# Kernel tuning notes

Hardware: AMD Instinct MI355X
Metric: run time of the kernel (lower is better)

## Reference

```python
import jax, jax.numpy as jnp
import numpy as np

H, W, D = 512, 512, 16
THETA_ALPHA, THETA_BETA, THETA_GAMMA = 160.0, 3.0, 3.0
NUM_ITERS = 5
SPATIAL_RADIUS = 9      # ~3*theta_gamma truncation for the Gaussian spatial kernel
BILATERAL_RADIUS = 2    # small window stand-in for the permutohedral bilateral filter


def _gauss1d(sigma, radius):
    x = jnp.arange(-radius, radius + 1, dtype=jnp.float32)
    return jnp.exp(-(x * x) / (2.0 * sigma * sigma))  # unnormalized; norm-vals divide cancels scale


def spatial_filter(x):
    # x: (d, h, w) -> depthwise separable Gaussian blur with sigma = theta_gamma
    k = _gauss1d(THETA_GAMMA, SPATIAL_RADIUS)
    xi = x[:, None]  # (d, 1, h, w): d acts as batch, single channel
    kh = k.reshape(1, 1, -1, 1)
    kw = k.reshape(1, 1, 1, -1)
    y = jax.lax.conv_general_dilated(xi, kh, (1, 1), [(SPATIAL_RADIUS, SPATIAL_RADIUS), (0, 0)])
    y = jax.lax.conv_general_dilated(y, kw, (1, 1), [(0, 0), (SPATIAL_RADIUS, SPATIAL_RADIUS)])
    return y[:, 0]


def bilateral_filter(x, rgb):
    # x: (d, h, w), rgb: (3, h, w). Windowed bilateral (joint spatial/color Gaussian),
    # a dense stand-in for the permutohedral-lattice high_dim_filter custom op.
    d, h, w = x.shape
    r = BILATERAL_RADIUS
    xp = jnp.pad(x, ((0, 0), (r, r), (r, r)))
    rp = jnp.pad(rgb, ((0, 0), (r, r), (r, r)))
    vp = jnp.pad(jnp.ones((h, w), x.dtype), ((r, r), (r, r)))
    inv2a = 1.0 / (2.0 * THETA_ALPHA * THETA_ALPHA)
    inv2b = 1.0 / (2.0 * THETA_BETA * THETA_BETA)
    out = jnp.zeros_like(x)
    for dy in range(-r, r + 1):
        for dx in range(-r, r + 1):  # fixed small offset set, not a data-dim loop
            xs = xp[:, r + dy:r + dy + h, r + dx:r + dx + w]
            rs = rp[:, r + dy:r + dy + h, r + dx:r + dx + w]
            vs = vp[r + dy:r + dy + h, r + dx:r + dx + w]
            wgt = jnp.exp(-(dy * dy + dx * dx) * inv2a
                          - jnp.sum((rgb - rs) ** 2, axis=0) * inv2b) * vs
            out = out + wgt[None] * xs
    return out


def setup_inputs() -> dict:
    key = jax.random.key(0)
    ks = jax.random.split(key, 8)
    eye = jnp.eye(D, dtype=jnp.float32)
    return {
        "image": jax.random.uniform(ks[0], (1, H, W, 3), jnp.float32) * 255.0,
        "unaries_box": jax.random.normal(ks[1], (1, D, H, W), jnp.float32),
        "unaries_global": jax.random.normal(ks[2], (1, D, H, W), jnp.float32),
        "spatial_ker_weights": eye + 0.05 * jax.random.normal(ks[3], (D, D), jnp.float32),
        "bilateral_ker_weights": eye + 0.05 * jax.random.normal(ks[4], (D, D), jnp.float32),
        "compatibility_matrix": -eye + 0.05 * jax.random.normal(ks[5], (D, D), jnp.float32),
        "box_weight": jax.random.uniform(ks[6], (1,), jnp.float32),
        "global_weight": jax.random.uniform(ks[7], (1,), jnp.float32),
    }


def reference(image, unaries_box, unaries_global, spatial_ker_weights,
              bilateral_ker_weights, compatibility_matrix, box_weight, global_weight):
    unaries = unaries_box[0] * box_weight + unaries_global[0] * global_weight  # (d, h, w)
    rgb = jnp.transpose(image[0], (2, 0, 1))  # (3, h, w)

    ones = jnp.ones((D, H, W), jnp.float32)
    spatial_norm = spatial_filter(ones)
    bilateral_norm = bilateral_filter(ones, rgb)

    q = unaries
    for _ in range(NUM_ITERS):
        p = jax.nn.softmax(q, axis=0)                       # over detections
        sp = spatial_filter(p) / spatial_norm
        bl = bilateral_filter(p, rgb) / bilateral_norm
        msg = (jnp.einsum('ij,jhw->ihw', spatial_ker_weights, sp)
               + jnp.einsum('ij,jhw->ihw', bilateral_ker_weights, bl))
        pairwise = jnp.einsum('ij,jhw->ihw', compatibility_matrix, msg)
        q = unaries - pairwise

    return jnp.transpose(q, (1, 2, 0))[None]  # (1, h, w, d)
```

## Files before the change

kernel.cpp:

```cpp
#include <hip/hip_runtime.h>


constexpr int H = 512, W = 512;
constexpr int HW = H * W;
constexpr int NUM_ITERS = 5;
constexpr float INV2A = 1.0f / (2.0f * 160.0f * 160.0f);
constexpr float INV2B = 1.0f / (2.0f * 3.0f * 3.0f);

constexpr size_t PLANAR_F = (size_t)HW * 8;
constexpr size_t OFF_U  = 0;
constexpr size_t OFF_PA = OFF_U  + (size_t)HW * 16;
constexpr size_t OFF_PB = OFF_PA + PLANAR_F;
constexpr size_t OFF_T  = OFF_PB + PLANAR_F;
constexpr size_t OFF_SV = OFF_T  + PLANAR_F;
constexpr size_t OFF_KG = OFF_SV + 512;
constexpr size_t OFF_M1 = OFF_KG + 32;
constexpr size_t OFF_M2 = OFF_M1 + 256;

__device__ inline void unpack2(unsigned u, float& lo, float& hi) {
    lo = __uint_as_float(u << 16);
    hi = __uint_as_float(u & 0xFFFF0000u);
}
__device__ inline unsigned short f2bf(float x) {
    unsigned u = __float_as_uint(x);
    return (unsigned short)((u + 0x7FFFu + ((u >> 16) & 1u)) >> 16);
}
__device__ inline unsigned pack2(float a, float b) {
    return (unsigned)f2bf(a) | ((unsigned)f2bf(b) << 16);
}
__device__ inline int swz8(int b, int per) { return (b & 7) * per + (b >> 3); }

__global__ void k_init(const float* __restrict__ Sw, const float* __restrict__ Bw,
                       const float* __restrict__ Cm, float* __restrict__ ws) {
    __shared__ float kg[19];
    int tid = threadIdx.x;
    if (tid < 19) { int t = tid - 9; kg[tid] = expf(-(float)(t * t) / 18.0f); }
    __syncthreads();
    if (tid < 19) ws[OFF_KG + tid] = kg[tid];
    if (tid < 512) {
        float s = 0.0f;
        for (int t = -9; t <= 9; ++t) {
            int yy = tid + t;
            if (yy >= 0 && yy < 512) s += kg[t + 9];
        }
        ws[OFF_SV + tid] = s;
    }
    if (tid < 256) {
        int r = tid >> 4, c = tid & 15;
        float a = 0.0f, b = 0.0f;
        for (int k = 0; k < 16; ++k) {
            float cv = Cm[r * 16 + k];
            a += cv * Sw[k * 16 + c];
            b += cv * Bw[k * 16 + c];
        }
        ws[OFF_M1 + tid] = a;
        ws[OFF_M2 + tid] = b;
    }
}

__global__ __launch_bounds__(256) void k_prep(const float* __restrict__ ub,
                                              const float* __restrict__ ug,
                                              const float* __restrict__ pbw,
                                              const float* __restrict__ pgw,
                                              float* __restrict__ ws) {
    int pix = blockIdx.x * 256 + threadIdx.x;
    float bw = pbw[0], gw = pgw[0];

    float u[16];
#pragma unroll
    for (int i = 0; i < 16; ++i)
        u[i] = ub[(size_t)i * HW + pix] * bw + ug[(size_t)i * HW + pix] * gw;

    float4* U4 = (float4*)(ws + OFF_U);
#pragma unroll
    for (int j = 0; j < 4; ++j)
        U4[(size_t)pix * 4 + j] = make_float4(u[4 * j], u[4 * j + 1], u[4 * j + 2], u[4 * j + 3]);

    float m = u[0];
#pragma unroll
    for (int i = 1; i < 16; ++i) m = fmaxf(m, u[i]);
    float sum = 0.0f;
#pragma unroll
    for (int i = 0; i < 16; ++i) { u[i] = __expf(u[i] - m); sum += u[i]; }
    float inv = 1.0f / sum;
    uint2* PA = (uint2*)(ws + OFF_PA);
#pragma unroll
    for (int q = 0; q < 4; ++q)
        PA[(size_t)q * HW + pix] = make_uint2(pack2(u[4 * q] * inv, u[4 * q + 1] * inv),
                                              pack2(u[4 * q + 2] * inv, u[4 * q + 3] * inv));
}

__global__ __launch_bounds__(256) void k_convv(const float* __restrict__ ws,
                                               const uint2* __restrict__ P,
                                               uint2* __restrict__ T) {
    int b = swz8(blockIdx.x, 128);
    int gtid = b * 256 + threadIdx.x;
    int x  = gtid & 511;
    int q  = (gtid >> 9) & 3;
    int yb = (gtid >> 11) << 2;

    float kg[19];
#pragma unroll
    for (int t = 0; t < 19; ++t) kg[t] = ws[OFF_KG + t];

    const uint2* Pq = P + (size_t)q * HW;
    float4 acc[4];
#pragma unroll
    for (int k = 0; k < 4; ++k) acc[k] = make_float4(0.f, 0.f, 0.f, 0.f);

#pragma unroll
    for (int t = 0; t < 22; ++t) {
        int yy = yb + t - 9;
        float4 p = make_float4(0.f, 0.f, 0.f, 0.f);
        if ((unsigned)yy < (unsigned)H) {
            uint2 v = Pq[(size_t)yy * W + x];
            unpack2(v.x, p.x, p.y);
            unpack2(v.y, p.z, p.w);
        }
        int k0 = (t - 18 > 0) ? t - 18 : 0;
        int k1 = (t < 3) ? t : 3;
#pragma unroll
        for (int k = k0; k <= k1; ++k) {
            float w = kg[t - k];
            acc[k].x += w * p.x; acc[k].y += w * p.y;
            acc[k].z += w * p.z; acc[k].w += w * p.w;
        }
    }
    uint2* Tq = T + (size_t)q * HW;
#pragma unroll
    for (int k = 0; k < 4; ++k)
        Tq[(size_t)(yb + k) * W + x] = make_uint2(pack2(acc[k].x, acc[k].y),
                                                  pack2(acc[k].z, acc[k].w));
}

__global__ __launch_bounds__(256) void k_combine(const float* __restrict__ ws,
                                                 const float* __restrict__ img,
                                                 const uint2* __restrict__ Tsrc,
                                                 const uint2* __restrict__ Psrc,
                                                 uint2* __restrict__ Pdst,
                                                 float4* __restrict__ outF,
                                                 int do_softmax) {
    __shared__ uint2 sT[4 * 4 * 82];
    __shared__ uint2 sP[4 * 8 * 68];
    __shared__ float sI[8 * 68 * 3];
    __shared__ float skg[19];
    __shared__ float sM1[256], sM2[256];

    int tid = threadIdx.x;
    int b = swz8(blockIdx.x, 128);
    int x0 = (b & 7) * 64;
    int y0 = (b >> 3) * 4;

    if (tid < 19) skg[tid] = ws[OFF_KG + tid];
    sM1[tid] = ws[OFF_M1 + tid];
    sM2[tid] = ws[OFF_M2 + tid];

    for (int e = tid; e < 1312; e += 256) {
        int q = e / 328, rem = e - q * 328;
        int row = rem / 82, px = rem - row * 82;
        int gx = x0 - 9 + px;
        uint2 v = make_uint2(0u, 0u);
        if ((unsigned)gx < (unsigned)W)
            v = Tsrc[(size_t)q * HW + (size_t)(y0 + row) * W + gx];
        sT[e] = v;
    }
    for (int e = tid; e < 2176; e += 256) {
        int q = e / 544, rem = e - q * 544;
        int row = rem / 68, px = rem - row * 68;
        int gx = x0 - 2 + px, gy = y0 - 2 + row;
        uint2 v = make_uint2(0u, 0u);
        if ((unsigned)gx < (unsigned)W && (unsigned)gy < (unsigned)H)
            v = Psrc[(size_t)q * HW + (size_t)gy * W + gx];
        sP[e] = v;
    }
    for (int e = tid; e < 544; e += 256) {
        int row = e / 68, px = e - row * 68;
        int gx = x0 - 2 + px, gy = y0 - 2 + row;
        float r = 0.f, g = 0.f, bb = 0.f;
        if ((unsigned)gx < (unsigned)W && (unsigned)gy < (unsigned)H) {
            const float* ip = img + ((size_t)gy * W + gx) * 3;
            r = ip[0]; g = ip[1]; bb = ip[2];
        }
        sI[e * 3 + 0] = r; sI[e * 3 + 1] = g; sI[e * 3 + 2] = bb;
    }
    __syncthreads();

    int ly = tid >> 6, lx = tid & 63;
    int y = y0 + ly, x = x0 + lx;

    float qn[16];

    {
        float sp[16];
#pragma unroll
        for (int i = 0; i < 16; ++i) sp[i] = 0.0f;
#pragma unroll
        for (int t = 0; t < 19; ++t) {
            float k = skg[t];
            int base = ly * 82 + lx + t;
#pragma unroll
            for (int q = 0; q < 4; ++q) {
                uint2 v = sT[q * 328 + base];
                float a, bq, c, d;
                unpack2(v.x, a, bq); unpack2(v.y, c, d);
                sp[4 * q + 0] += k * a; sp[4 * q + 1] += k * bq;
                sp[4 * q + 2] += k * c; sp[4 * q + 3] += k * d;
            }
        }
        float inv_sn = 1.0f / (ws[OFF_SV + y] * ws[OFF_SV + x]);
#pragma unroll
        for (int i = 0; i < 16; ++i) sp[i] *= inv_sn;
#pragma unroll
        for (int i = 0; i < 16; ++i) {
            float acc = 0.0f;
#pragma unroll
            for (int j4 = 0; j4 < 4; ++j4) {
                float4 m1 = *(const float4*)&sM1[i * 16 + j4 * 4];
                acc += m1.x * sp[4 * j4 + 0] + m1.y * sp[4 * j4 + 1]
                     + m1.z * sp[4 * j4 + 2] + m1.w * sp[4 * j4 + 3];
            }
            qn[i] = -acc;
        }
    }

    {
        float bl[16];
#pragma unroll
        for (int i = 0; i < 16; ++i) bl[i] = 0.0f;
        float bn = 0.0f;
        const float* ic = &sI[((ly + 2) * 68 + lx + 2) * 3];
        float r0 = ic[0], g0 = ic[1], b0 = ic[2];
#pragma unroll
        for (int dy = 0; dy < 5; ++dy) {
            int gy = y + dy - 2;
            bool vy = (unsigned)gy < (unsigned)H;
#pragma unroll
            for (int dx = 0; dx < 5; ++dx) {
                int gx = x + dx - 2;
                const float* ip = &sI[((ly + dy) * 68 + lx + dx) * 3];
                float dr = r0 - ip[0], dg = g0 - ip[1], db = b0 - ip[2];
                float wgt = __expf(-(float)((dy - 2) * (dy - 2) + (dx - 2) * (dx - 2)) * INV2A
                                   - (dr * dr + dg * dg + db * db) * INV2B);
                if (!(vy && (unsigned)gx < (unsigned)W)) wgt = 0.0f;
                bn += wgt;
                int base = (ly + dy) * 68 + lx + dx;
#pragma unroll
                for (int q = 0; q < 4; ++q) {
                    uint2 v = sP[q * 544 + base];
                    float a, bq, c, d;
                    unpack2(v.x, a, bq); unpack2(v.y, c, d);
                    bl[4 * q + 0] += wgt * a; bl[4 * q + 1] += wgt * bq;
                    bl[4 * q + 2] += wgt * c; bl[4 * q + 3] += wgt * d;
                }
            }
        }
        float inv_bn = 1.0f / bn;
#pragma unroll
        for (int i = 0; i < 16; ++i) bl[i] *= inv_bn;
#pragma unroll
        for (int i = 0; i < 16; ++i) {
            float acc = 0.0f;
#pragma unroll
            for (int j4 = 0; j4 < 4; ++j4) {
                float4 m2 = *(const float4*)&sM2[i * 16 + j4 * 4];
                acc += m2.x * bl[4 * j4 + 0] + m2.y * bl[4 * j4 + 1]
                     + m2.z * bl[4 * j4 + 2] + m2.w * bl[4 * j4 + 3];
            }
            qn[i] -= acc;
        }
    }

    size_t pix = (size_t)y * W + x;
    const float4* U4 = (const float4*)(ws + OFF_U);
#pragma unroll
    for (int j = 0; j < 4; ++j) {
        float4 u = U4[pix * 4 + j];
        qn[4 * j + 0] += u.x; qn[4 * j + 1] += u.y;
        qn[4 * j + 2] += u.z; qn[4 * j + 3] += u.w;
    }

    if (do_softmax) {
        float m = qn[0];
#pragma unroll
        for (int i = 1; i < 16; ++i) m = fmaxf(m, qn[i]);
        float sum = 0.0f;
#pragma unroll
        for (int i = 0; i < 16; ++i) { qn[i] = __expf(qn[i] - m); sum += qn[i]; }
        float inv = 1.0f / sum;
#pragma unroll
        for (int q = 0; q < 4; ++q)
            Pdst[(size_t)q * HW + pix] = make_uint2(pack2(qn[4 * q] * inv, qn[4 * q + 1] * inv),
                                                    pack2(qn[4 * q + 2] * inv, qn[4 * q + 3] * inv));
    } else {
#pragma unroll
        for (int j = 0; j < 4; ++j)
            outF[pix * 4 + j] = make_float4(qn[4 * j], qn[4 * j + 1], qn[4 * j + 2], qn[4 * j + 3]);
    }
}

extern "C" void kernel_launch(void* const* d_in, const int* in_sizes, int n_in,
                              void* d_out, int out_size, void* d_ws, size_t ws_size,
                              hipStream_t stream) {
    const float* img = (const float*)d_in[0];
    const float* ub  = (const float*)d_in[1];
    const float* ug  = (const float*)d_in[2];
    const float* Sw  = (const float*)d_in[3];
    const float* Bw  = (const float*)d_in[4];
    const float* Cm  = (const float*)d_in[5];
    const float* pbw = (const float*)d_in[6];
    const float* pgw = (const float*)d_in[7];
    float* ws  = (float*)d_ws;
    float* out = (float*)d_out;

    uint2* PA = (uint2*)(ws + OFF_PA);
    uint2* PB = (uint2*)(ws + OFF_PB);
    uint2* T  = (uint2*)(ws + OFF_T);

    k_init<<<1, 512, 0, stream>>>(Sw, Bw, Cm, ws);
    k_prep<<<HW / 256, 256, 0, stream>>>(ub, ug, pbw, pgw, ws);

    for (int it = 0; it < NUM_ITERS; ++it) {
        uint2* Ps = (it & 1) ? PB : PA;
        uint2* Pd = (it & 1) ? PA : PB;
        k_convv<<<1024, 256, 0, stream>>>(ws, Ps, T);
        if (it < NUM_ITERS - 1)
            k_combine<<<1024, 256, 0, stream>>>(ws, img, T, Ps, Pd, nullptr, 1);
        else
            k_combine<<<1024, 256, 0, stream>>>(ws, img, T, Ps, nullptr, (float4*)out, 0);
    }
}
```

Measured before the change: 303.6 us.

## Store unaries as planar bf16 and prefetch bilateral tiles into registers during spatial pass

Unaries are stored as planar bf16 pairs instead of fp32 float4, which halves the bytes k_combine reads for them each iteration. k_combine now issues the global loads for the P halo and image halo into registers before the spatial stage. It writes them to shared memory only after that stage, and the unary load is also issued early, so load latency can overlap the spatial accumulation. The cost is extra registers (pR, iR, uR) that may lower occupancy, plus an extra __syncthreads, and bf16 unaries lose precision.

```diff
diff --git a/kernel.cpp b/kernel.cpp
--- a/kernel.cpp
+++ b/kernel.cpp
@@ -9,7 +9,7 @@
 
 constexpr size_t PLANAR_F = (size_t)HW * 8;
 constexpr size_t OFF_U  = 0;
-constexpr size_t OFF_PA = OFF_U  + (size_t)HW * 16;
+constexpr size_t OFF_PA = OFF_U  + PLANAR_F;
 constexpr size_t OFF_PB = OFF_PA + PLANAR_F;
 constexpr size_t OFF_T  = OFF_PB + PLANAR_F;
 constexpr size_t OFF_SV = OFF_T  + PLANAR_F;
@@ -71,10 +71,11 @@
     for (int i = 0; i < 16; ++i)
         u[i] = ub[(size_t)i * HW + pix] * bw + ug[(size_t)i * HW + pix] * gw;
 
-    float4* U4 = (float4*)(ws + OFF_U);
-#pragma unroll
-    for (int j = 0; j < 4; ++j)
-        U4[(size_t)pix * 4 + j] = make_float4(u[4 * j], u[4 * j + 1], u[4 * j + 2], u[4 * j + 3]);
+    uint2* Uq = (uint2*)(ws + OFF_U);
+#pragma unroll
+    for (int q = 0; q < 4; ++q)
+        Uq[(size_t)q * HW + pix] = make_uint2(pack2(u[4 * q], u[4 * q + 1]),
+                                              pack2(u[4 * q + 2], u[4 * q + 3]));
 
     float m = u[0];
 #pragma unroll
@@ -137,6 +138,7 @@
                                                  const float* __restrict__ img,
                                                  const uint2* __restrict__ Tsrc,
                                                  const uint2* __restrict__ Psrc,
+                                                 const uint2* __restrict__ Usrc,
                                                  uint2* __restrict__ Pdst,
                                                  float4* __restrict__ outF,
                                                  int do_softmax) {
@@ -155,6 +157,33 @@
     sM1[tid] = ws[OFF_M1 + tid];
     sM2[tid] = ws[OFF_M2 + tid];
 
+    uint2 pR[9];
+#pragma unroll
+    for (int k = 0; k < 9; ++k) {
+        int e = tid + (k << 8);
+        pR[k] = make_uint2(0u, 0u);
+        if (e < 2176) {
+            int q = e / 544, rem = e - q * 544;
+            int row = rem / 68, px = rem - row * 68;
+            int gx = x0 - 2 + px, gy = y0 - 2 + row;
+            if ((unsigned)gx < (unsigned)W && (unsigned)gy < (unsigned)H)
+                pR[k] = Psrc[(size_t)q * HW + (size_t)gy * W + gx];
+        }
+    }
+    float iR[3][3];
+#pragma unroll
+    for (int k = 0; k < 3; ++k) {
+        int e = tid + (k << 8);
+        iR[k][0] = iR[k][1] = iR[k][2] = 0.f;
+        if (e < 544) {
+            int row = e / 68, px = e - row * 68;
+            int gx = x0 - 2 + px, gy = y0 - 2 + row;
+            if ((unsigned)gx < (unsigned)W && (unsigned)gy < (unsigned)H) {
+                const float* ip = img + ((size_t)gy * W + gx) * 3;
+                iR[k][0] = ip[0]; iR[k][1] = ip[1]; iR[k][2] = ip[2];
+            }
+        }
+    }
     for (int e = tid; e < 1312; e += 256) {
         int q = e / 328, rem = e - q * 328;
         int row = rem / 82, px = rem - row * 82;
@@ -164,32 +193,13 @@
             v = Tsrc[(size_t)q * HW + (size_t)(y0 + row) * W + gx];
         sT[e] = v;
     }
-    for (int e = tid; e < 2176; e += 256) {
-        int q = e / 544, rem = e - q * 544;
-        int row = rem / 68, px = rem - row * 68;
-        int gx = x0 - 2 + px, gy = y0 - 2 + row;
-        uint2 v = make_uint2(0u, 0u);
-        if ((unsigned)gx < (unsigned)W && (unsigned)gy < (unsigned)H)
-            v = Psrc[(size_t)q * HW + (size_t)gy * W + gx];
-        sP[e] = v;
-    }
-    for (int e = tid; e < 544; e += 256) {
-        int row = e / 68, px = e - row * 68;
-        int gx = x0 - 2 + px, gy = y0 - 2 + row;
-        float r = 0.f, g = 0.f, bb = 0.f;
-        if ((unsigned)gx < (unsigned)W && (unsigned)gy < (unsigned)H) {
-            const float* ip = img + ((size_t)gy * W + gx) * 3;
-            r = ip[0]; g = ip[1]; bb = ip[2];
-        }
-        sI[e * 3 + 0] = r; sI[e * 3 + 1] = g; sI[e * 3 + 2] = bb;
-    }
     __syncthreads();
 
     int ly = tid >> 6, lx = tid & 63;
     int y = y0 + ly, x = x0 + lx;
+    size_t pix = (size_t)y * W + x;
 
     float qn[16];
-
     {
         float sp[16];
 #pragma unroll
@@ -222,6 +232,26 @@
             qn[i] = -acc;
         }
     }
+
+    __syncthreads();
+#pragma unroll
+    for (int k = 0; k < 9; ++k) {
+        int e = tid + (k << 8);
+        if (e < 2176) sP[e] = pR[k];
+    }
+#pragma unroll
+    for (int k = 0; k < 3; ++k) {
+        int e = tid + (k << 8);
+        if (e < 544) {
+            sI[e * 3 + 0] = iR[k][0];
+            sI[e * 3 + 1] = iR[k][1];
+            sI[e * 3 + 2] = iR[k][2];
+        }
+    }
+    uint2 uR[4];
+#pragma unroll
+    for (int q = 0; q < 4; ++q) uR[q] = Usrc[(size_t)q * HW + pix];
+    __syncthreads();
 
     {
         float bl[16];
@@ -270,13 +300,12 @@
         }
     }
 
-    size_t pix = (size_t)y * W + x;
-    const float4* U4 = (const float4*)(ws + OFF_U);
-#pragma unroll
-    for (int j = 0; j < 4; ++j) {
-        float4 u = U4[pix * 4 + j];
-        qn[4 * j + 0] += u.x; qn[4 * j + 1] += u.y;
-        qn[4 * j + 2] += u.z; qn[4 * j + 3] += u.w;
+#pragma unroll
+    for (int q = 0; q < 4; ++q) {
+        float a, bq, c, d;
+        unpack2(uR[q].x, a, bq); unpack2(uR[q].y, c, d);
+        qn[4 * q + 0] += a; qn[4 * q + 1] += bq;
+        qn[4 * q + 2] += c; qn[4 * q + 3] += d;
     }
 
     if (do_softmax) {
@@ -312,6 +341,7 @@
     float* ws  = (float*)d_ws;
     float* out = (float*)d_out;
 
+    uint2* U  = (uint2*)(ws + OFF_U);
     uint2* PA = (uint2*)(ws + OFF_PA);
     uint2* PB = (uint2*)(ws + OFF_PB);
     uint2* T  = (uint2*)(ws + OFF_T);
@@ -324,8 +354,8 @@
         uint2* Pd = (it & 1) ? PA : PB;
         k_convv<<<1024, 256, 0, stream>>>(ws, Ps, T);
         if (it < NUM_ITERS - 1)
-            k_combine<<<1024, 256, 0, stream>>>(ws, img, T, Ps, Pd, nullptr, 1);
+            k_combine<<<1024, 256, 0, stream>>>(ws, img, T, Ps, U, Pd, nullptr, 1);
         else
-            k_combine<<<1024, 256, 0, stream>>>(ws, img, T, Ps, nullptr, (float4*)out, 0);
-    }
-}
+            k_combine<<<1024, 256, 0, stream>>>(ws, img, T, Ps, U, nullptr, (float4*)out, 0);
+    }
+}
```

Measured after the change: 401.9 us. +32.4%, slower.
